# Kernel optimization log

Measured on AMD Instinct MI355X. Metric: run time of the kernel, lower is better.

Reference implementation:

```python
import jax, jax.numpy as jnp
import numpy as np
import math

P = 7          # patch / kernel size (must be odd for onion-peeling: N = 1+4*m*(m+1) = P*P)
EPS = 1e-6
EPS_W = 0.5

def _ball_dirs():
    u = [np.array([[1.0, 0.0]])]
    s = [np.zeros(1)]
    for k in range(1, P // 2 + 1):
        n = 8 * k
        th = np.linspace(0.0, 2.0 * math.pi * (1.0 - 1.0 / n), n)
        u.append(np.stack([np.cos(th), np.sin(th)], 1))
        s.append(np.full(n, k / (P // 2)))
    return (np.concatenate(u, 0).astype(np.float32), np.concatenate(s).astype(np.float32))

_U, _S = _ball_dirs()  # [N,2], [N], N == P*P == 49

def _forward(x, metric_w, metric_b, proj_w, proj_b):
    B, C, H, W = x.shape
    Hp, Wp = H // P, W // P
    u = jnp.asarray(_U)
    s = jnp.asarray(_S)
    # metric net: strided conv -> 7 params per patch
    params = jax.lax.conv_general_dilated(
        x, metric_w, (P, P), 'VALID',
        dimension_numbers=('NCHW', 'OIHW', 'NCHW')) + metric_b[None, :, None, None]
    v_raw = jnp.moveaxis(params[:, :2], 1, -1)                      # [B,Hp,Wp,2]
    v = v_raw / jnp.maximum(jnp.linalg.norm(v_raw, axis=-1, keepdims=True), 1e-12)
    eig = 2.0 * jax.nn.sigmoid(jnp.moveaxis(params[:, 2:4], 1, -1))  # [B,Hp,Wp,2]
    scale = 0.5 + 1.5 * jax.nn.sigmoid(jnp.moveaxis(params[:, 4:5], 1, -1))
    eig = eig * scale
    vp = jnp.stack([-v[..., 1], v[..., 0]], -1)
    R = jnp.stack([v, vp], -1)                                      # [B,Hp,Wp,2,2] (columns v, v_perp)
    M = R @ (eig[..., None] * jnp.swapaxes(R, -1, -2))              # R diag(eig) R^T
    w = params[:, 5:7]                                              # [B,2,Hp,Wp]
    w = w * (1.0 - EPS_W) * jax.nn.sigmoid(jnp.linalg.norm(w, axis=1, keepdims=True))
    # Finsler-Randers norm F(u) = sqrt(u^T M u + eps) + w.u for all N unit dirs
    quad = jnp.einsum('nj,bhwij,ni->bnhw', u, M, u)                 # [B,N,Hp,Wp]
    drift = jnp.einsum('bihw,ni->bnhw', w, u)
    F_u = jnp.sqrt(quad + EPS) + drift
    y = (u[None, :, :, None, None] / (F_u[:, :, None] + EPS)
         * s[None, :, None, None, None])                            # [B,N,2,Hp,Wp]
    y = y.reshape(B, P, P, 2, Hp, Wp)[:, :, :, ::-1]                # flip last coord pair (x,y)->(y,x)
    gi = jnp.arange(P, dtype=x.dtype) - P // 2
    grid = jnp.stack(jnp.meshgrid(gi, gi, indexing='ij'), -1)       # [P,P,2]
    off = y - grid[None, :, :, :, None, None]                       # [B,P,P,2,Hp,Wp]
    off_y = jnp.transpose(off[:, :, :, 0], (0, 3, 4, 1, 2))         # [B,Hp,Wp,P,P]
    off_x = jnp.transpose(off[:, :, :, 1], (0, 3, 4, 1, 2))
    base_h = (jnp.arange(Hp, dtype=x.dtype) * P)[None, :, None, None, None]
    base_w = (jnp.arange(Wp, dtype=x.dtype) * P)[None, None, :, None, None]
    ki = jnp.arange(P, dtype=x.dtype)
    py = off_y + base_h + ki[None, None, None, :, None]             # sample rows
    px = off_x + base_w + ki[None, None, None, None, :]             # sample cols
    # bilinear sampling with zero padding (torchvision deform_conv2d semantics)
    y0 = jnp.floor(py)
    x0 = jnp.floor(px)
    wy = py - y0
    wx = px - x0

    def gather(yi, xi):
        valid = (yi >= 0) & (yi <= H - 1) & (xi >= 0) & (xi <= W - 1)
        yc = jnp.clip(yi, 0, H - 1).astype(jnp.int32)
        xc = jnp.clip(xi, 0, W - 1).astype(jnp.int32)
        vals = jax.vmap(lambda img, yy, xx: img[:, yy, xx])(x, yc, xc)  # [B,C,Hp,Wp,P,P]
        return vals * valid[:, None].astype(x.dtype)

    sampled = (gather(y0, x0) * ((1 - wy) * (1 - wx))[:, None]
               + gather(y0, x0 + 1) * ((1 - wy) * wx)[:, None]
               + gather(y0 + 1, x0) * (wy * (1 - wx))[:, None]
               + gather(y0 + 1, x0 + 1) * (wy * wx)[:, None])       # [B,C,Hp,Wp,P,P]
    out = jnp.einsum('bchwij,ecij->behw', sampled, proj_w) + proj_b[None, :, None, None]
    return jnp.moveaxis(out.reshape(B, out.shape[1], -1), 1, 2)     # [B, Hp*Wp, E]

def setup_inputs():
    key = jax.random.key(0)
    k0, k1, k2 = jax.random.split(key, 3)
    B, C, H, W, E = 64, 3, 224, 224, 384
    x = jax.random.normal(k0, (B, C, H, W), jnp.float32)
    metric_w = jax.random.normal(k1, (7, C, P, P), jnp.float32) / math.sqrt(C * P * P)
    metric_b = jnp.zeros((7,), jnp.float32)
    proj_w = jax.random.normal(k2, (E, C, P, P), jnp.float32) / (P * math.sqrt(C))
    proj_b = jnp.zeros((E,), jnp.float32)
    return {"x": x, "metric_w": metric_w, "metric_b": metric_b,
            "proj_w": proj_w, "proj_b": proj_b}

def reference(x, metric_w, metric_b, proj_w, proj_b):
    return _forward(x, metric_w, metric_b, proj_w, proj_b)
```

## Files before the change

### kernel.cpp

```cpp
#include <hip/hip_runtime.h>
#include <math.h>

#define PP   7
#define NDIR 49
#define CIN  3
#define KK   147
#define KPAD 160
#define EE   384
#define HH   224
#define WW   224
#define GG   16
#define TB   256
#define SSTR 17
#define NPX  112

typedef __attribute__((ext_vector_type(8))) __bf16 bf16x8;
typedef __attribute__((ext_vector_type(4))) float  f32x4;

__device__ __forceinline__ float sigmoidf_(float v) {
    return 1.0f / (1.0f + expf(-v));
}

__global__ void pack_pw_kernel(const float* __restrict__ pw, unsigned short* __restrict__ pwB) {
    int idx = blockIdx.x * blockDim.x + threadIdx.x;
    if (idx < EE * KPAD) {
        int e = idx / KPAD;
        int k = idx - e * KPAD;
        float v = (k < KK) ? pw[e * KK + k] : 0.0f;
        __bf16 h = (__bf16)v;
        pwB[idx] = *(unsigned short*)&h;
    }
}

__launch_bounds__(TB, 6)
__global__ void fused_kernel(const float* __restrict__ x,
                             const float* __restrict__ mw,
                             const float* __restrict__ mb,
                             const unsigned short* __restrict__ pwB,
                             const float* __restrict__ pb,
                             float* __restrict__ out) {
    __shared__ float mws[7 * KK];
    __shared__ float dirs[NDIR][3];
    __shared__ float par_s[GG][8];
    __shared__ float der_s[GG][5];
    __shared__ __align__(16) float buf[2512];

    const int t   = threadIdx.x;
    const int blk = blockIdx.x;
    const int b   = blk >> 6;
    const int rem = blk & 63;
    const int hp  = rem >> 1;
    const int wp0 = (rem & 1) * GG;
    const size_t m0 = (size_t)blk * GG;
    const int row0 = hp * PP;
    const int col0 = wp0 * PP;

    const float* xb = x + (size_t)b * (CIN * HH * WW);

    for (int i = t; i < 7 * KK; i += TB) mws[i] = mw[i];
    if (t >= 64 && t < 64 + NDIR) {
        int n = t - 64;
        float u0, u1, s;
        if (n == 0)      { u0 = 1.0f; u1 = 0.0f; s = 0.0f; }
        else if (n < 9)  { float th = (float)(n - 1)  * 0.78539816339744831f; u0 = cosf(th); u1 = sinf(th); s = 0.33333334f; }
        else if (n < 25) { float th = (float)(n - 9)  * 0.39269908169872414f; u0 = cosf(th); u1 = sinf(th); s = 0.66666669f; }
        else             { float th = (float)(n - 25) * 0.26179938779914941f; u0 = cosf(th); u1 = sinf(th); s = 1.0f; }
        dirs[n][0] = u0; dirs[n][1] = u1; dirs[n][2] = s;
    }

    for (int item = t; item < CIN * 7 * NPX; item += TB) {
        int c = item / (7 * NPX), r2 = item - c * (7 * NPX);
        int i = r2 / NPX, px = r2 - i * NPX;
        buf[item] = xb[(size_t)c * (HH * WW) + (size_t)(row0 + i) * WW + col0 + px];
    }
    __syncthreads();

    if (t < 112) {
        int prm = t >> 4, g = t & 15;
        const float* wrow = &mws[prm * KK];
        float acc0 = 0.0f, acc1 = 0.0f, acc2 = 0.0f;
        #pragma unroll 1
        for (int i = 0; i < 7; ++i) {
            const float* b0 = &buf[(0 * 7 + i) * NPX + g * 7];
            const float* b1 = &buf[(1 * 7 + i) * NPX + g * 7];
            const float* b2 = &buf[(2 * 7 + i) * NPX + g * 7];
            const float* w0 = &wrow[i * 7];
            const float* w1 = &wrow[49 + i * 7];
            const float* w2 = &wrow[98 + i * 7];
            #pragma unroll
            for (int j = 0; j < 7; ++j) {
                acc0 = fmaf(b0[j], w0[j], acc0);
                acc1 = fmaf(b1[j], w1[j], acc1);
                acc2 = fmaf(b2[j], w2[j], acc2);
            }
        }
        par_s[g][prm] = mb[prm] + acc0 + acc1 + acc2;
    }
    __syncthreads();

    if (t < GG) {
        float a0 = par_s[t][0], a1 = par_s[t][1], a2 = par_s[t][2], a3 = par_s[t][3];
        float a4 = par_s[t][4], a5 = par_s[t][5], a6 = par_s[t][6];
        float nrm = sqrtf(a0 * a0 + a1 * a1);
        float inv = 1.0f / fmaxf(nrm, 1e-12f);
        float v0 = a0 * inv, v1 = a1 * inv;
        float e0 = 2.0f * sigmoidf_(a2);
        float e1 = 2.0f * sigmoidf_(a3);
        float sc = 0.5f + 1.5f * sigmoidf_(a4);
        e0 *= sc; e1 *= sc;
        float wn  = sqrtf(a5 * a5 + a6 * a6);
        float wsc = 0.5f * sigmoidf_(wn);
        der_s[t][0] = e0 * v0 * v0 + e1 * v1 * v1;
        der_s[t][1] = (e0 - e1) * v0 * v1;
        der_s[t][2] = e0 * v1 * v1 + e1 * v0 * v0;
        der_s[t][3] = a5 * wsc;
        der_s[t][4] = a6 * wsc;
    }
    __syncthreads();

    #pragma unroll
    for (int rep = 0; rep < 4; ++rep) {
        int item = rep * TB + t;
        if (item < GG * NDIR) {
            int g = item / NDIR;
            int n = item - g * NDIR;
            float u0 = dirs[n][0], u1 = dirs[n][1], s = dirs[n][2];
            float M00 = der_s[g][0], M01 = der_s[g][1], M11 = der_s[g][2];
            float w0 = der_s[g][3], w1 = der_s[g][4];
            float quad  = u0 * u0 * M00 + 2.0f * u0 * u1 * M01 + u1 * u1 * M11;
            float drift = w0 * u0 + w1 * u1;
            float F = sqrtf(quad + 1e-6f) + drift;
            float r = s / (F + 1e-6f);
            float py = (float)(row0 + 3) + u1 * r;
            float px = (float)(col0 + g * PP + 3) + u0 * r;
            float y0f = floorf(py), x0f = floorf(px);
            float y1f = y0f + 1.0f, x1f = x0f + 1.0f;
            float wy = py - y0f, wx = px - x0f;
            float c00 = (1.0f - wy) * (1.0f - wx);
            float c01 = (1.0f - wy) * wx;
            float c10 = wy * (1.0f - wx);
            float c11 = wy * wx;
            bool vy0 = (y0f >= 0.0f) && (y0f <= (float)(HH - 1));
            bool vy1 = (y1f >= 0.0f) && (y1f <= (float)(HH - 1));
            bool vx0 = (x0f >= 0.0f) && (x0f <= (float)(WW - 1));
            bool vx1 = (x1f >= 0.0f) && (x1f <= (float)(WW - 1));
            c00 *= (vy0 && vx0) ? 1.0f : 0.0f;
            c01 *= (vy0 && vx1) ? 1.0f : 0.0f;
            c10 *= (vy1 && vx0) ? 1.0f : 0.0f;
            c11 *= (vy1 && vx1) ? 1.0f : 0.0f;
            int iy0 = (int)fminf(fmaxf(y0f, 0.0f), (float)(HH - 1));
            int iy1 = (int)fminf(fmaxf(y1f, 0.0f), (float)(HH - 1));
            int ix0 = (int)fminf(fmaxf(x0f, 0.0f), (float)(WW - 1));
            int ix1 = (int)fminf(fmaxf(x1f, 0.0f), (float)(WW - 1));
            int o00 = iy0 * WW + ix0, o01 = iy0 * WW + ix1;
            int o10 = iy1 * WW + ix0, o11 = iy1 * WW + ix1;
            #pragma unroll
            for (int c = 0; c < CIN; ++c) {
                const float* xc = xb + c * (HH * WW);
                float v00 = xc[o00], v01 = xc[o01], v10 = xc[o10], v11 = xc[o11];
                buf[(c * NDIR + n) * SSTR + g] =
                    v00 * c00 + v01 * c01 + v10 * c10 + v11 * c11;
            }
        }
    }
    __syncthreads();

    const int lane = t & 63;
    const int wv   = t >> 6;
    const int nrow = lane & 15;
    const int hi   = lane >> 4;

    bf16x8 sfr[5];
    #pragma unroll
    for (int ks = 0; ks < 5; ++ks) {
        #pragma unroll
        for (int j = 0; j < 8; ++j) {
            int k = ks * 32 + hi * 8 + j;
            float v = (k < KK) ? buf[k * SSTR + nrow] : 0.0f;
            sfr[ks][j] = (__bf16)v;
        }
    }

    float* orow = out + (m0 + nrow) * EE;
    #pragma unroll
    for (int q = 0; q < 6; ++q) {
        int tile = wv * 6 + q;
        int erow = tile * 16 + nrow;
        const unsigned short* arow = pwB + (size_t)erow * KPAD + hi * 8;
        f32x4 acc = {0.0f, 0.0f, 0.0f, 0.0f};
        #pragma unroll
        for (int ks = 0; ks < 5; ++ks) {
            bf16x8 afr = *(const bf16x8*)&arow[ks * 32];
            acc = __builtin_amdgcn_mfma_f32_16x16x32_bf16(afr, sfr[ks], acc, 0, 0, 0);
        }
        int e0 = tile * 16 + hi * 4;
        f32x4 b4 = *(const f32x4*)&pb[e0];
        f32x4 o = acc + b4;
        *(f32x4*)&orow[e0] = o;
    }
}

extern "C" void kernel_launch(void* const* d_in, const int* in_sizes, int n_in,
                              void* d_out, int out_size, void* d_ws, size_t ws_size,
                              hipStream_t stream) {
    const float* x  = (const float*)d_in[0];
    const float* mw = (const float*)d_in[1];
    const float* mb = (const float*)d_in[2];
    const float* pw = (const float*)d_in[3];
    const float* pb = (const float*)d_in[4];
    float* out = (float*)d_out;

    unsigned short* pwB = (unsigned short*)d_ws;

    const int B = in_sizes[0] / (CIN * HH * WW);

    pack_pw_kernel<<<(EE * KPAD + 255) / 256, 256, 0, stream>>>(pw, pwB);
    fused_kernel<<<B * 64, TB, 0, stream>>>(x, mw, mb, pwB, pb, out);
}
```

Baseline: 214.9 us.

## Repack input to interleaved RGBX layout for vectorized bilinear gathers

Adds a pre-pass that converts the planar NCHW input into a pixel-interleaved float4 (RGB plus pad) buffer in workspace, so each bilinear corner fetch becomes one 16-byte load instead of three scattered scalar loads. The fused kernel now stages its patch rows and issues its gathers from this layout, two samples per thread at a time so more loads are in flight. This costs an extra full read of the input and a write of a buffer about 4/3 its size every call, plus more shared memory. A fallback planar kernel runs when the workspace is too small.

```diff
diff --git a/kernel.cpp b/kernel.cpp
--- a/kernel.cpp
+++ b/kernel.cpp
@@ -21,7 +21,11 @@
     return 1.0f / (1.0f + expf(-v));
 }
 
-__global__ void pack_pw_kernel(const float* __restrict__ pw, unsigned short* __restrict__ pwB) {
+__global__ void pack_kernel(const float* __restrict__ x,
+                            const float* __restrict__ pw,
+                            float* __restrict__ xp,
+                            unsigned short* __restrict__ pwB,
+                            int npix4) {
     int idx = blockIdx.x * blockDim.x + threadIdx.x;
     if (idx < EE * KPAD) {
         int e = idx / KPAD;
@@ -30,10 +34,65 @@
         __bf16 h = (__bf16)v;
         pwB[idx] = *(unsigned short*)&h;
     }
+    if (idx < npix4) {
+        const int ppi = HH * WW / 4;
+        int b = idx / ppi;
+        int p = (idx - b * ppi) * 4;
+        const float* xb = x + (size_t)b * (CIN * HH * WW) + p;
+        f32x4 r0 = *(const f32x4*)(xb);
+        f32x4 r1 = *(const f32x4*)(xb + HH * WW);
+        f32x4 r2 = *(const f32x4*)(xb + 2 * HH * WW);
+        float* op = xp + ((size_t)b * (HH * WW) + p) * 4;
+        #pragma unroll
+        for (int i = 0; i < 4; ++i) {
+            f32x4 v = {r0[i], r1[i], r2[i], 0.0f};
+            *(f32x4*)(op + i * 4) = v;
+        }
+    }
+}
+
+__device__ __forceinline__ void geom_(int item, int row0, int col0,
+                                      const float dirs[NDIR][3], const float der[GG][5],
+                                      int& g, int& n,
+                                      int& o00, int& o01, int& o10, int& o11,
+                                      float& c00, float& c01, float& c10, float& c11) {
+    g = item / NDIR;
+    n = item - g * NDIR;
+    float u0 = dirs[n][0], u1 = dirs[n][1], s = dirs[n][2];
+    float M00 = der[g][0], M01 = der[g][1], M11 = der[g][2];
+    float w0 = der[g][3], w1 = der[g][4];
+    float quad  = u0 * u0 * M00 + 2.0f * u0 * u1 * M01 + u1 * u1 * M11;
+    float drift = w0 * u0 + w1 * u1;
+    float F = sqrtf(quad + 1e-6f) + drift;
+    float r = s / (F + 1e-6f);
+    float py = (float)(row0 + 3) + u1 * r;
+    float px = (float)(col0 + g * PP + 3) + u0 * r;
+    float y0f = floorf(py), x0f = floorf(px);
+    float y1f = y0f + 1.0f, x1f = x0f + 1.0f;
+    float wy = py - y0f, wx = px - x0f;
+    c00 = (1.0f - wy) * (1.0f - wx);
+    c01 = (1.0f - wy) * wx;
+    c10 = wy * (1.0f - wx);
+    c11 = wy * wx;
+    bool vy0 = (y0f >= 0.0f) && (y0f <= (float)(HH - 1));
+    bool vy1 = (y1f >= 0.0f) && (y1f <= (float)(HH - 1));
+    bool vx0 = (x0f >= 0.0f) && (x0f <= (float)(WW - 1));
+    bool vx1 = (x1f >= 0.0f) && (x1f <= (float)(WW - 1));
+    c00 *= (vy0 && vx0) ? 1.0f : 0.0f;
+    c01 *= (vy0 && vx1) ? 1.0f : 0.0f;
+    c10 *= (vy1 && vx0) ? 1.0f : 0.0f;
+    c11 *= (vy1 && vx1) ? 1.0f : 0.0f;
+    int iy0 = (int)fminf(fmaxf(y0f, 0.0f), (float)(HH - 1));
+    int iy1 = (int)fminf(fmaxf(y1f, 0.0f), (float)(HH - 1));
+    int ix0 = (int)fminf(fmaxf(x0f, 0.0f), (float)(WW - 1));
+    int ix1 = (int)fminf(fmaxf(x1f, 0.0f), (float)(WW - 1));
+    o00 = iy0 * WW + ix0; o01 = iy0 * WW + ix1;
+    o10 = iy1 * WW + ix0; o11 = iy1 * WW + ix1;
 }
 
 __launch_bounds__(TB, 6)
 __global__ void fused_kernel(const float* __restrict__ x,
+                             const float* __restrict__ xp,
                              const float* __restrict__ mw,
                              const float* __restrict__ mb,
                              const unsigned short* __restrict__ pwB,
@@ -43,7 +102,7 @@
     __shared__ float dirs[NDIR][3];
     __shared__ float par_s[GG][8];
     __shared__ float der_s[GG][5];
-    __shared__ __align__(16) float buf[2512];
+    __shared__ __align__(16) float buf[3136];
 
     const int t   = threadIdx.x;
     const int blk = blockIdx.x;
@@ -55,8 +114,6 @@
     const int row0 = hp * PP;
     const int col0 = wp0 * PP;
 
-    const float* xb = x + (size_t)b * (CIN * HH * WW);
-
     for (int i = t; i < 7 * KK; i += TB) mws[i] = mw[i];
     if (t >= 64 && t < 64 + NDIR) {
         int n = t - 64;
@@ -68,10 +125,11 @@
         dirs[n][0] = u0; dirs[n][1] = u1; dirs[n][2] = s;
     }
 
-    for (int item = t; item < CIN * 7 * NPX; item += TB) {
-        int c = item / (7 * NPX), r2 = item - c * (7 * NPX);
-        int i = r2 / NPX, px = r2 - i * NPX;
-        buf[item] = xb[(size_t)c * (HH * WW) + (size_t)(row0 + i) * WW + col0 + px];
+    const size_t pbase = (size_t)b * (HH * WW);
+    for (int item = t; item < 7 * NPX; item += TB) {
+        int i = item / NPX, px = item - i * NPX;
+        f32x4 v = *(const f32x4*)(xp + (pbase + (size_t)(row0 + i) * WW + col0 + px) * 4);
+        *(f32x4*)&buf[item * 4] = v;
     }
     __syncthreads();
 
@@ -81,17 +139,15 @@
         float acc0 = 0.0f, acc1 = 0.0f, acc2 = 0.0f;
         #pragma unroll 1
         for (int i = 0; i < 7; ++i) {
-            const float* b0 = &buf[(0 * 7 + i) * NPX + g * 7];
-            const float* b1 = &buf[(1 * 7 + i) * NPX + g * 7];
-            const float* b2 = &buf[(2 * 7 + i) * NPX + g * 7];
+            const float* bp = &buf[(i * NPX + g * 7) * 4];
             const float* w0 = &wrow[i * 7];
             const float* w1 = &wrow[49 + i * 7];
             const float* w2 = &wrow[98 + i * 7];
             #pragma unroll
             for (int j = 0; j < 7; ++j) {
-                acc0 = fmaf(b0[j], w0[j], acc0);
-                acc1 = fmaf(b1[j], w1[j], acc1);
-                acc2 = fmaf(b2[j], w2[j], acc2);
+                acc0 = fmaf(bp[j * 4 + 0], w0[j], acc0);
+                acc1 = fmaf(bp[j * 4 + 1], w1[j], acc1);
+                acc2 = fmaf(bp[j * 4 + 2], w2[j], acc2);
             }
         }
         par_s[g][prm] = mb[prm] + acc0 + acc1 + acc2;
@@ -119,47 +175,36 @@
     __syncthreads();
 
     #pragma unroll
-    for (int rep = 0; rep < 4; ++rep) {
-        int item = rep * TB + t;
-        if (item < GG * NDIR) {
-            int g = item / NDIR;
-            int n = item - g * NDIR;
-            float u0 = dirs[n][0], u1 = dirs[n][1], s = dirs[n][2];
-            float M00 = der_s[g][0], M01 = der_s[g][1], M11 = der_s[g][2];
-            float w0 = der_s[g][3], w1 = der_s[g][4];
-            float quad  = u0 * u0 * M00 + 2.0f * u0 * u1 * M01 + u1 * u1 * M11;
-            float drift = w0 * u0 + w1 * u1;
-            float F = sqrtf(quad + 1e-6f) + drift;
-            float r = s / (F + 1e-6f);
-            float py = (float)(row0 + 3) + u1 * r;
-            float px = (float)(col0 + g * PP + 3) + u0 * r;
-            float y0f = floorf(py), x0f = floorf(px);
-            float y1f = y0f + 1.0f, x1f = x0f + 1.0f;
-            float wy = py - y0f, wx = px - x0f;
-            float c00 = (1.0f - wy) * (1.0f - wx);
-            float c01 = (1.0f - wy) * wx;
-            float c10 = wy * (1.0f - wx);
-            float c11 = wy * wx;
-            bool vy0 = (y0f >= 0.0f) && (y0f <= (float)(HH - 1));
-            bool vy1 = (y1f >= 0.0f) && (y1f <= (float)(HH - 1));
-            bool vx0 = (x0f >= 0.0f) && (x0f <= (float)(WW - 1));
-            bool vx1 = (x1f >= 0.0f) && (x1f <= (float)(WW - 1));
-            c00 *= (vy0 && vx0) ? 1.0f : 0.0f;
-            c01 *= (vy0 && vx1) ? 1.0f : 0.0f;
-            c10 *= (vy1 && vx0) ? 1.0f : 0.0f;
-            c11 *= (vy1 && vx1) ? 1.0f : 0.0f;
-            int iy0 = (int)fminf(fmaxf(y0f, 0.0f), (float)(HH - 1));
-            int iy1 = (int)fminf(fmaxf(y1f, 0.0f), (float)(HH - 1));
-            int ix0 = (int)fminf(fmaxf(x0f, 0.0f), (float)(WW - 1));
-            int ix1 = (int)fminf(fmaxf(x1f, 0.0f), (float)(WW - 1));
-            int o00 = iy0 * WW + ix0, o01 = iy0 * WW + ix1;
-            int o10 = iy1 * WW + ix0, o11 = iy1 * WW + ix1;
+    for (int half = 0; half < 2; ++half) {
+        int itemA = half * 512 + t;
+        int itemB = itemA + 256;
+        bool validB = (itemB < GG * NDIR);
+        int itemBc = validB ? itemB : 0;
+
+        int gA, nA, a00, a01, a10, a11;  float cA00, cA01, cA10, cA11;
+        int gB, nB, b00, b01, b10, b11;  float cB00, cB01, cB10, cB11;
+        geom_(itemA,  row0, col0, dirs, der_s, gA, nA, a00, a01, a10, a11, cA00, cA01, cA10, cA11);
+        geom_(itemBc, row0, col0, dirs, der_s, gB, nB, b00, b01, b10, b11, cB00, cB01, cB10, cB11);
+
+        f32x4 qa0 = *(const f32x4*)(xp + (pbase + (size_t)a00) * 4);
+        f32x4 qa1 = *(const f32x4*)(xp + (pbase + (size_t)a01) * 4);
+        f32x4 qa2 = *(const f32x4*)(xp + (pbase + (size_t)a10) * 4);
+        f32x4 qa3 = *(const f32x4*)(xp + (pbase + (size_t)a11) * 4);
+        f32x4 qb0 = *(const f32x4*)(xp + (pbase + (size_t)b00) * 4);
+        f32x4 qb1 = *(const f32x4*)(xp + (pbase + (size_t)b01) * 4);
+        f32x4 qb2 = *(const f32x4*)(xp + (pbase + (size_t)b10) * 4);
+        f32x4 qb3 = *(const f32x4*)(xp + (pbase + (size_t)b11) * 4);
+
+        #pragma unroll
+        for (int c = 0; c < CIN; ++c) {
+            buf[(c * NDIR + nA) * SSTR + gA] =
+                qa0[c] * cA00 + qa1[c] * cA01 + qa2[c] * cA10 + qa3[c] * cA11;
+        }
+        if (validB) {
             #pragma unroll
             for (int c = 0; c < CIN; ++c) {
-                const float* xc = xb + c * (HH * WW);
-                float v00 = xc[o00], v01 = xc[o01], v10 = xc[o10], v11 = xc[o11];
-                buf[(c * NDIR + n) * SSTR + g] =
-                    v00 * c00 + v01 * c01 + v10 * c10 + v11 * c11;
+                buf[(c * NDIR + nB) * SSTR + gB] =
+                    qb0[c] * cB00 + qb1[c] * cB01 + qb2[c] * cB10 + qb3[c] * cB11;
             }
         }
     }
@@ -181,6 +226,128 @@
         }
     }
 
+    float* orow = out + (m0 + nrow) * EE;
+    #pragma unroll
+    for (int q = 0; q < 6; ++q) {
+        int tile = wv * 6 + q;
+        int erow = tile * 16 + nrow;
+        const unsigned short* arow = pwB + (size_t)erow * KPAD + hi * 8;
+        f32x4 acc = {0.0f, 0.0f, 0.0f, 0.0f};
+        #pragma unroll
+        for (int ks = 0; ks < 5; ++ks) {
+            bf16x8 afr = *(const bf16x8*)&arow[ks * 32];
+            acc = __builtin_amdgcn_mfma_f32_16x16x32_bf16(afr, sfr[ks], acc, 0, 0, 0);
+        }
+        int e0 = tile * 16 + hi * 4;
+        f32x4 b4 = *(const f32x4*)&pb[e0];
+        f32x4 o = acc + b4;
+        *(f32x4*)&orow[e0] = o;
+    }
+}
+
+__launch_bounds__(TB, 6)
+__global__ void fused_planar_kernel(const float* __restrict__ x,
+                                    const float* __restrict__ mw,
+                                    const float* __restrict__ mb,
+                                    const unsigned short* __restrict__ pwB,
+                                    const float* __restrict__ pb,
+                                    float* __restrict__ out) {
+    __shared__ float mws[7 * KK];
+    __shared__ float dirs[NDIR][3];
+    __shared__ float par_s[GG][8];
+    __shared__ float der_s[GG][5];
+    __shared__ __align__(16) float buf[2512];
+
+    const int t   = threadIdx.x;
+    const int blk = blockIdx.x;
+    const int b   = blk >> 6;
+    const int rem = blk & 63;
+    const int hp  = rem >> 1;
+    const int wp0 = (rem & 1) * GG;
+    const size_t m0 = (size_t)blk * GG;
+    const int row0 = hp * PP;
+    const int col0 = wp0 * PP;
+    const float* xb = x + (size_t)b * (CIN * HH * WW);
+
+    for (int i = t; i < 7 * KK; i += TB) mws[i] = mw[i];
+    if (t >= 64 && t < 64 + NDIR) {
+        int n = t - 64;
+        float u0, u1, s;
+        if (n == 0)      { u0 = 1.0f; u1 = 0.0f; s = 0.0f; }
+        else if (n < 9)  { float th = (float)(n - 1)  * 0.78539816339744831f; u0 = cosf(th); u1 = sinf(th); s = 0.33333334f; }
+        else if (n < 25) { float th = (float)(n - 9)  * 0.39269908169872414f; u0 = cosf(th); u1 = sinf(th); s = 0.66666669f; }
+        else             { float th = (float)(n - 25) * 0.26179938779914941f; u0 = cosf(th); u1 = sinf(th); s = 1.0f; }
+        dirs[n][0] = u0; dirs[n][1] = u1; dirs[n][2] = s;
+    }
+    for (int item = t; item < CIN * 7 * NPX; item += TB) {
+        int c = item / (7 * NPX), r2 = item - c * (7 * NPX);
+        int i = r2 / NPX, px = r2 - i * NPX;
+        buf[item] = xb[(size_t)c * (HH * WW) + (size_t)(row0 + i) * WW + col0 + px];
+    }
+    __syncthreads();
+    if (t < 112) {
+        int prm = t >> 4, g = t & 15;
+        const float* wrow = &mws[prm * KK];
+        float acc0 = 0.0f, acc1 = 0.0f, acc2 = 0.0f;
+        #pragma unroll 1
+        for (int i = 0; i < 7; ++i) {
+            const float* b0 = &buf[(0 * 7 + i) * NPX + g * 7];
+            const float* b1 = &buf[(1 * 7 + i) * NPX + g * 7];
+            const float* b2 = &buf[(2 * 7 + i) * NPX + g * 7];
+            #pragma unroll
+            for (int j = 0; j < 7; ++j) {
+                acc0 = fmaf(b0[j], wrow[i * 7 + j], acc0);
+                acc1 = fmaf(b1[j], wrow[49 + i * 7 + j], acc1);
+                acc2 = fmaf(b2[j], wrow[98 + i * 7 + j], acc2);
+            }
+        }
+        par_s[g][prm] = mb[prm] + acc0 + acc1 + acc2;
+    }
+    __syncthreads();
+    if (t < GG) {
+        float a0 = par_s[t][0], a1 = par_s[t][1], a2 = par_s[t][2], a3 = par_s[t][3];
+        float a4 = par_s[t][4], a5 = par_s[t][5], a6 = par_s[t][6];
+        float nrm = sqrtf(a0 * a0 + a1 * a1);
+        float inv = 1.0f / fmaxf(nrm, 1e-12f);
+        float v0 = a0 * inv, v1 = a1 * inv;
+        float e0 = 2.0f * sigmoidf_(a2);
+        float e1 = 2.0f * sigmoidf_(a3);
+        float sc = 0.5f + 1.5f * sigmoidf_(a4);
+        e0 *= sc; e1 *= sc;
+        float wn  = sqrtf(a5 * a5 + a6 * a6);
+        float wsc = 0.5f * sigmoidf_(wn);
+        der_s[t][0] = e0 * v0 * v0 + e1 * v1 * v1;
+        der_s[t][1] = (e0 - e1) * v0 * v1;
+        der_s[t][2] = e0 * v1 * v1 + e1 * v0 * v0;
+        der_s[t][3] = a5 * wsc;
+        der_s[t][4] = a6 * wsc;
+    }
+    __syncthreads();
+    for (int item = t; item < GG * NDIR; item += TB) {
+        int g, n, o00, o01, o10, o11; float c00, c01, c10, c11;
+        geom_(item, row0, col0, dirs, der_s, g, n, o00, o01, o10, o11, c00, c01, c10, c11);
+        #pragma unroll
+        for (int c = 0; c < CIN; ++c) {
+            const float* xc = xb + c * (HH * WW);
+            buf[(c * NDIR + n) * SSTR + g] =
+                xc[o00] * c00 + xc[o01] * c01 + xc[o10] * c10 + xc[o11] * c11;
+        }
+    }
+    __syncthreads();
+    const int lane = t & 63;
+    const int wv   = t >> 6;
+    const int nrow = lane & 15;
+    const int hi   = lane >> 4;
+    bf16x8 sfr[5];
+    #pragma unroll
+    for (int ks = 0; ks < 5; ++ks) {
+        #pragma unroll
+        for (int j = 0; j < 8; ++j) {
+            int k = ks * 32 + hi * 8 + j;
+            float v = (k < KK) ? buf[k * SSTR + nrow] : 0.0f;
+            sfr[ks][j] = (__bf16)v;
+        }
+    }
     float* orow = out + (m0 + nrow) * EE;
     #pragma unroll
     for (int q = 0; q < 6; ++q) {
@@ -211,9 +378,20 @@
     float* out = (float*)d_out;
 
     unsigned short* pwB = (unsigned short*)d_ws;
+    float* xp = (float*)((char*)d_ws + (size_t)(1 << 17));
 
     const int B = in_sizes[0] / (CIN * HH * WW);
-
-    pack_pw_kernel<<<(EE * KPAD + 255) / 256, 256, 0, stream>>>(pw, pwB);
-    fused_kernel<<<B * 64, TB, 0, stream>>>(x, mw, mb, pwB, pb, out);
-}
+    const int npix = B * HH * WW;
+    const int npix4 = npix / 4;
+    const size_t need = (size_t)(1 << 17) + (size_t)npix * 4 * sizeof(float);
+    const bool packed = ws_size >= need;
+
+    if (packed) {
+        int grid = (npix4 > EE * KPAD ? npix4 : EE * KPAD);
+        pack_kernel<<<(grid + 255) / 256, 256, 0, stream>>>(x, pw, xp, pwB, npix4);
+        fused_kernel<<<B * 64, TB, 0, stream>>>(x, xp, mw, mb, pwB, pb, out);
+    } else {
+        pack_kernel<<<(EE * KPAD + 255) / 256, 256, 0, stream>>>(x, pw, xp, pwB, 0);
+        fused_planar_kernel<<<B * 64, TB, 0, stream>>>(x, mw, mb, pwB, pb, out);
+    }
+}
```

After: 206.1 us. 1.04x faster.
